# Kernel tuning notes

Measured on AMD Instinct MI355X. Metric: run time of the kernel, lower is better.

The kernel has to match this reference:

```python
import jax, jax.numpy as jnp
import numpy as np
import math

B, S, D, H = 2, 2048, 1024, 16
HD = D // H  # 64


def setup_inputs() -> dict:
    key = jax.random.key(0)
    ks = jax.random.split(key, 7)
    scale = 1.0 / math.sqrt(D)
    return {
        "hidden_states": jax.random.normal(ks[0], (B, S, D), jnp.float32),
        "attention_mask": jnp.zeros((B, 1, 1, S), jnp.int32),  # 0 = valid (code negates .bool())
        "Wq": jax.random.normal(ks[1], (D, D), jnp.float32) * scale,
        "bq": jnp.zeros((D,), jnp.float32),
        "Wk": jax.random.normal(ks[2], (D, D), jnp.float32) * scale,
        "bk": jnp.zeros((D,), jnp.float32),
        "Wv": jax.random.normal(ks[3], (D, D), jnp.float32) * scale,
        "bv": jnp.zeros((D,), jnp.float32),
    }


def reference(hidden_states, attention_mask, Wq, bq, Wk, bk, Wv, bv):
    b, s, d = hidden_states.shape

    def proj(W, bias):
        # torch Linear: x @ W.T + b ; weight shape [out, in]
        y = jnp.einsum('bsd,ed->bse', hidden_states, W) + bias
        return y.reshape(b, s, H, HD).transpose(0, 2, 1, 3)  # b h s d

    q, k, v = proj(Wq, bq), proj(Wk, bk), proj(Wv, bv)

    scores = jnp.einsum('bhqd,bhkd->bhqk', q, k) * (1.0 / math.sqrt(HD))
    causal = jnp.tril(jnp.ones((s, s), bool))[None, None]          # [1,1,S,S]
    pad = ~(attention_mask.astype(bool))                           # [B,1,1,S], True = valid
    mask = causal & pad
    scores = jnp.where(mask, scores, -jnp.inf)
    probs = jax.nn.softmax(scores, axis=-1)  # dropout prob = 0.0 -> identity
    out = jnp.einsum('bhqk,bhkd->bhqd', probs, v)
    return out.transpose(0, 2, 1, 3).reshape(b, s, d)
```

## Files before the change

kernel.cpp:

```cpp
#include <hip/hip_runtime.h>

typedef __bf16 bf16;
typedef __bf16 bf16x4 __attribute__((ext_vector_type(4)));
typedef __bf16 bf16x8 __attribute__((ext_vector_type(8)));
typedef float f32x4 __attribute__((ext_vector_type(4)));
typedef float f32x16 __attribute__((ext_vector_type(16)));
typedef unsigned u32x4 __attribute__((ext_vector_type(4)));

#define DEV __device__ __forceinline__

typedef const __attribute__((address_space(1))) void gvoid_t;
typedef __attribute__((address_space(3))) void lvoid_t;

DEV void gload_lds16(const void* g, void* l) {
  __builtin_amdgcn_global_load_lds((gvoid_t*)g, (lvoid_t*)l, 16, 0, 0);
}

DEV f32x4 mfma16(bf16x8 a, bf16x8 b, f32x4 c) {
  return __builtin_amdgcn_mfma_f32_16x16x32_bf16(a, b, c, 0, 0, 0);
}
DEV f32x16 mfma32(bf16x8 a, bf16x8 b, f32x16 c) {
  return __builtin_amdgcn_mfma_f32_32x32x16_bf16(a, b, c, 0, 0, 0);
}

DEV unsigned pk2(float lo, float hi) {
  unsigned r;
  asm("v_cvt_pk_bf16_f32 %0, %1, %2" : "=v"(r) : "v"(lo), "v"(hi));
  return r;
}

#define QSCALE 0.18033688011112042f

__global__ __launch_bounds__(256) void cvt_all(
    const float* __restrict__ hs, const float* __restrict__ Wq,
    const float* __restrict__ Wk, const float* __restrict__ Wv,
    bf16* __restrict__ Xb, bf16* __restrict__ Wb) {
  const int i = blockIdx.x * 256 + threadIdx.x;
  const float* src;
  bf16* dst;
  int off;
  if (i < 1048576) {
    src = hs; dst = Xb; off = i;
  } else {
    const int j = i - 1048576;
    const int sel = j >> 18;
    off = j & 262143;
    src = (sel == 0) ? Wq : (sel == 1) ? Wk : Wv;
    dst = Wb + (size_t)sel * 1048576;
  }
  float4 f = reinterpret_cast<const float4*>(src)[off];
  bf16x4 o;
  o[0] = (bf16)f.x; o[1] = (bf16)f.y; o[2] = (bf16)f.z; o[3] = (bf16)f.w;
  reinterpret_cast<bf16x4*>(dst)[off] = o;
}

__global__ __launch_bounds__(256) void gemm_qkv(
    const bf16* __restrict__ X, const bf16* __restrict__ W,
    const float* __restrict__ bq, const float* __restrict__ bk,
    const float* __restrict__ bv,
    bf16* __restrict__ Q, bf16* __restrict__ Kf, bf16* __restrict__ Vf) {
  __shared__ bf16 As[128 * 64];
  __shared__ bf16 Bs[128 * 64];
  const int t = threadIdx.x;
  const int lane = t & 63, w = t >> 6;
  const int wr = w >> 1, wc = w & 1;
  const int bid = blockIdx.x;
  const int swzb = (bid & 7) * 96 + (bid >> 3);
  const int m0 = (swzb / 24) * 128;
  const int n0 = (swzb % 24) * 128;
  const int cl = lane & 15, g8 = (lane >> 4) * 8;

  f32x4 acc[4][4];
  for (int mi = 0; mi < 4; ++mi)
    for (int ni = 0; ni < 4; ++ni)
      for (int r = 0; r < 4; ++r) acc[mi][ni][r] = 0.0f;

  for (int k0 = 0; k0 < 1024; k0 += 64) {
#pragma unroll
    for (int i = 0; i < 4; ++i) {
      int c = i * 256 + t;
      int row = c >> 3, col8 = (c & 7) * 8;
      gload_lds16(X + (size_t)(m0 + row) * 1024 + k0 + col8, As + c * 8);
      gload_lds16(W + (size_t)(n0 + row) * 1024 + k0 + col8, Bs + c * 8);
    }
    __syncthreads();
#pragma unroll
    for (int kk = 0; kk < 64; kk += 32) {
      bf16x8 a[4], b[4];
#pragma unroll
      for (int mi = 0; mi < 4; ++mi)
        a[mi] = *(const bf16x8*)&As[(wr * 64 + mi * 16 + cl) * 64 + kk + g8];
#pragma unroll
      for (int ni = 0; ni < 4; ++ni)
        b[ni] = *(const bf16x8*)&Bs[(wc * 64 + ni * 16 + cl) * 64 + kk + g8];
      __builtin_amdgcn_s_setprio(1);
#pragma unroll
      for (int mi = 0; mi < 4; ++mi)
#pragma unroll
        for (int ni = 0; ni < 4; ++ni)
          acc[mi][ni] = mfma16(a[mi], b[ni], acc[mi][ni]);
      __builtin_amdgcn_s_setprio(0);
    }
    __syncthreads();
  }

  const int rq = (lane >> 4) * 4;
#pragma unroll
  for (int mi = 0; mi < 4; ++mi) {
#pragma unroll
    for (int ni = 0; ni < 4; ++ni) {
      const int n = n0 + wc * 64 + ni * 16 + cl;
      const int mbase = m0 + wr * 64 + mi * 16 + rq;
      const int b = mbase >> 11, s0 = mbase & 2047;
      if (n < 1024) {
        const float bias = bq[n];
        const int h = n >> 6, hd = n & 63;
#pragma unroll
        for (int r = 0; r < 4; ++r)
          Q[(((size_t)(b * 16 + h)) * 2048 + s0 + r) * 64 + hd] =
              (bf16)((acc[mi][ni][r] + bias) * QSCALE);
      } else if (n < 2048) {
        const int n2 = n - 1024;
        const float bias = bk[n2];
        const int h = n2 >> 6, hd = n2 & 63;
        const int kt = s0 >> 6, half = (s0 >> 5) & 1, rr = s0 & 31;
        const size_t base =
            ((size_t)((b * 16 + h) * 32 + kt) * 8 + half * 4 + (hd >> 4)) * 512 +
            ((((hd >> 3) & 1) * 32 + rr) * 8 + (hd & 7));
#pragma unroll
        for (int r = 0; r < 4; ++r)
          Kf[base + r * 8] = (bf16)(acc[mi][ni][r] + bias);
      } else {
        const int n2 = n - 2048;
        const float bias = bv[n2];
        const int h = n2 >> 6, hd = n2 & 63;
        const int kt = s0 >> 6, half = (s0 >> 5) & 1;
        const int j = (s0 >> 4) & 1, hi2 = (s0 >> 3) & 1;
        const size_t idx =
            ((size_t)(((b * 16 + h) * 32 + kt) * 4 + half * 2 + j) * 2 +
             (hd >> 5)) * 512 +
            ((hi2 * 32 + (hd & 31)) * 8 + (s0 & 7));
        bf16x4 pk;
#pragma unroll
        for (int r = 0; r < 4; ++r) pk[r] = (bf16)(acc[mi][ni][r] + bias);
        *(bf16x4*)&Vf[idx] = pk;
      }
    }
  }
}

__global__ __launch_bounds__(256, 3) void flash_attn(
    const bf16* __restrict__ Q, const bf16* __restrict__ Kf,
    const bf16* __restrict__ Vf, const int* __restrict__ amask,
    float* __restrict__ out) {
  __shared__ float Oar[2][2048];
  __shared__ float Lar[2][32];
  __shared__ unsigned long long mk[32];
  const int t = threadIdx.x, lane = t & 63, w = t >> 6;
  const int bh = blockIdx.x & 31;
  const int p = blockIdx.x >> 5;
  const int b = bh >> 4, h = bh & 15;
  const int sub = w >> 1, par = w & 1;
  const int r31 = lane & 31, hi = lane >> 5;

  const bf16* Qp = Q + (size_t)bh * 2048 * 64;
  const bf16* Kfb = Kf + (size_t)bh * 32 * 4096 + lane * 8;
  const bf16* Vfb = Vf + (size_t)bh * 32 * 4096 + lane * 8;

#pragma unroll
  for (int i = 0; i < 8; ++i) {
    const int kt = w * 8 + i;
    const unsigned long long bal =
        __ballot(amask[b * 2048 + kt * 64 + lane] != 0);
    if (lane == 0) mk[kt] = bal;
  }
  __syncthreads();

  for (int sw = 0; sw < 2; ++sw) {
    const int qt = sw ? p : 31 - p;
    const int row0 = qt * 64 + sub * 32;
    bf16x8 qf[4];
#pragma unroll
    for (int hdk = 0; hdk < 4; ++hdk)
      qf[hdk] =
          *(const bf16x8*)&Qp[(size_t)(row0 + r31) * 64 + hdk * 16 + hi * 8];
    f32x16 o0, o1;
#pragma unroll
    for (int rg = 0; rg < 16; ++rg) { o0[rg] = 0.0f; o1[rg] = 0.0f; }
    float ls = 0.0f;

    for (int kt = par; kt <= qt; kt += 2) {
      const bf16* kb = Kfb + (size_t)kt * 4096;
      const bf16* vb = Vfb + (size_t)kt * 4096;
      bf16x8 kf[8], vf[8];
#pragma unroll
      for (int u = 0; u < 8; ++u) kf[u] = *(const bf16x8*)(kb + u * 512);
#pragma unroll
      for (int u = 0; u < 8; ++u) vf[u] = *(const bf16x8*)(vb + u * 512);
      const unsigned long long pb = mk[kt];
      const bool diag = (kt == qt);
      const bool domask = diag || (pb != 0ull);
      const int kv0 = kt * 64;
#pragma unroll
      for (int half = 0; half < 2; ++half) {
        f32x16 s4;
#pragma unroll
        for (int rg = 0; rg < 16; ++rg) s4[rg] = -12.0f;
        __builtin_amdgcn_s_setprio(1);
#pragma unroll
        for (int hdk = 0; hdk < 4; ++hdk)
          s4 = mfma32(kf[half * 4 + hdk], qf[hdk], s4);
        __builtin_amdgcn_s_setprio(0);
        if (domask) {
#pragma unroll
          for (int rg = 0; rg < 16; ++rg) {
            const int kvt = half * 32 + (rg & 3) + 8 * (rg >> 2) + 4 * hi;
            const bool bad = (diag && (kv0 + kvt > row0 + r31)) ||
                             ((pb >> kvt) & 1ull);
            s4[rg] = bad ? -1e30f : s4[rg];
          }
        }
        float pe[16];
#pragma unroll
        for (int rg = 0; rg < 16; ++rg) pe[rg] = exp2f(s4[rg]);
        ls += (((pe[0] + pe[1]) + (pe[2] + pe[3])) +
               ((pe[4] + pe[5]) + (pe[6] + pe[7]))) +
              (((pe[8] + pe[9]) + (pe[10] + pe[11])) +
               ((pe[12] + pe[13]) + (pe[14] + pe[15])));
#pragma unroll
        for (int j = 0; j < 2; ++j) {
          const unsigned a0 = pk2(pe[8 * j + 0], pe[8 * j + 1]);
          const unsigned a1 = pk2(pe[8 * j + 2], pe[8 * j + 3]);
          const unsigned b0 = pk2(pe[8 * j + 4], pe[8 * j + 5]);
          const unsigned b1 = pk2(pe[8 * j + 6], pe[8 * j + 7]);
          const unsigned xa0 = __shfl_xor(a0, 32, 64);
          const unsigned xa1 = __shfl_xor(a1, 32, 64);
          const unsigned xb0 = __shfl_xor(b0, 32, 64);
          const unsigned xb1 = __shfl_xor(b1, 32, 64);
          u32x4 wv;
          wv[0] = hi ? xb0 : a0;
          wv[1] = hi ? xb1 : a1;
          wv[2] = hi ? b0 : xa0;
          wv[3] = hi ? b1 : xa1;
          const bf16x8 paf = __builtin_bit_cast(bf16x8, wv);
          __builtin_amdgcn_s_setprio(1);
          o0 = mfma32(paf, vf[half * 4 + j * 2 + 0], o0);
          o1 = mfma32(paf, vf[half * 4 + j * 2 + 1], o1);
          __builtin_amdgcn_s_setprio(0);
        }
      }
    }

    ls += __shfl_xor(ls, 32, 64);
    if (par == 1) {
      float* Og = Oar[sub];
#pragma unroll
      for (int rg = 0; rg < 16; ++rg) {
        const int qrel = (rg & 3) + 8 * (rg >> 2) + 4 * hi;
        Og[qrel * 64 + r31] = o0[rg];
        Og[qrel * 64 + 32 + r31] = o1[rg];
      }
      if (lane < 32) Lar[sub][r31] = ls;
    }
    __syncthreads();
    if (par == 0) {
      const float lt = ls + Lar[sub][r31];
      const float inv = 1.0f / lt;
      const float* Og = Oar[sub];
#pragma unroll
      for (int rg = 0; rg < 16; ++rg) {
        const int qrel = (rg & 3) + 8 * (rg >> 2) + 4 * hi;
        const float invq = __shfl(inv, qrel, 64);
        float* op =
            &out[((size_t)b * 2048 + row0 + qrel) * 1024 + h * 64 + r31];
        op[0] = (o0[rg] + Og[qrel * 64 + r31]) * invq;
        op[32] = (o1[rg] + Og[qrel * 64 + 32 + r31]) * invq;
      }
    }
    __syncthreads();
  }
}

extern "C" void kernel_launch(void* const* d_in, const int* in_sizes, int n_in,
                              void* d_out, int out_size, void* d_ws,
                              size_t ws_size, hipStream_t stream) {
  const float* hs = (const float*)d_in[0];
  const int* amask = (const int*)d_in[1];
  const float* Wq = (const float*)d_in[2];
  const float* bq = (const float*)d_in[3];
  const float* Wk = (const float*)d_in[4];
  const float* bk = (const float*)d_in[5];
  const float* Wv = (const float*)d_in[6];
  const float* bv = (const float*)d_in[7];
  float* out = (float*)d_out;

  char* ws = (char*)d_ws;
  bf16* Xb = (bf16*)ws;
  bf16* Wb = (bf16*)(ws + 8ull * 1024 * 1024);
  bf16* Qb = (bf16*)(ws + 14ull * 1024 * 1024);
  bf16* Kfr = (bf16*)(ws + 22ull * 1024 * 1024);
  bf16* Vfr = (bf16*)(ws + 30ull * 1024 * 1024);

  cvt_all<<<7168, 256, 0, stream>>>(hs, Wq, Wk, Wv, Xb, Wb);
  gemm_qkv<<<768, 256, 0, stream>>>(Xb, Wb, bq, bk, bv, Qb, Kfr, Vfr);
  flash_attn<<<512, 256, 0, stream>>>(Qb, Kfr, Vfr, amask, out);
}
```

Baseline: 109.7 us.

## Split flash attention KV loop across four waves and double grid size

The attention kernel now gives each block one 32-row query sub-tile and splits the KV tiles across all four waves (stride 4) instead of two. The launch grows to 1024 blocks and occupancy is raised to 4 blocks per CU. Partial outputs are combined through a two-step LDS reduction. The bf16 P-matrix half swap now uses v_permlane32_swap instead of cross-lane shuffles, and exp2f is replaced by the hardware exp2 builtin. This trades more blocks and an extra reduction barrier for more parallelism over the causal KV range and fewer shuffle instructions.

Result: slower. 178.1 us (+62.4%).

```diff
diff --git a/kernel.cpp b/kernel.cpp
--- a/kernel.cpp
+++ b/kernel.cpp
@@ -27,6 +27,9 @@
   unsigned r;
   asm("v_cvt_pk_bf16_f32 %0, %1, %2" : "=v"(r) : "v"(lo), "v"(hi));
   return r;
+}
+DEV void plswap(unsigned& a, unsigned& b) {
+  asm("v_permlane32_swap_b32 %0, %1" : "+v"(a), "+v"(b));
 }
 
 #define QSCALE 0.18033688011112042f
@@ -149,7 +152,7 @@
   }
 }
 
-__global__ __launch_bounds__(256, 3) void flash_attn(
+__global__ __launch_bounds__(256, 4) void flash_attn(
     const bf16* __restrict__ Q, const bf16* __restrict__ Kf,
     const bf16* __restrict__ Vf, const int* __restrict__ amask,
     float* __restrict__ out) {
@@ -158,9 +161,9 @@
   __shared__ unsigned long long mk[32];
   const int t = threadIdx.x, lane = t & 63, w = t >> 6;
   const int bh = blockIdx.x & 31;
-  const int p = blockIdx.x >> 5;
+  const int p = (blockIdx.x >> 5) & 15;
+  const int sub = blockIdx.x >> 9;
   const int b = bh >> 4, h = bh & 15;
-  const int sub = w >> 1, par = w & 1;
   const int r31 = lane & 31, hi = lane >> 5;
 
   const bf16* Qp = Q + (size_t)bh * 2048 * 64;
@@ -176,6 +179,26 @@
   }
   __syncthreads();
 
+#define DUMPO(SL)                                                       \
+  do {                                                                  \
+    _Pragma("unroll") for (int rg = 0; rg < 16; ++rg) {                 \
+      const int qrel = (rg & 3) + 8 * (rg >> 2) + 4 * hi;               \
+      Oar[SL][qrel * 64 + r31] = o0[rg];                                \
+      Oar[SL][qrel * 64 + 32 + r31] = o1[rg];                           \
+    }                                                                   \
+    if (lane < 32) Lar[SL][r31] = ls;                                   \
+  } while (0)
+
+#define ADDO(SL)                                                        \
+  do {                                                                  \
+    _Pragma("unroll") for (int rg = 0; rg < 16; ++rg) {                 \
+      const int qrel = (rg & 3) + 8 * (rg >> 2) + 4 * hi;               \
+      o0[rg] += Oar[SL][qrel * 64 + r31];                               \
+      o1[rg] += Oar[SL][qrel * 64 + 32 + r31];                          \
+    }                                                                   \
+    ls += Lar[SL][r31];                                                 \
+  } while (0)
+
   for (int sw = 0; sw < 2; ++sw) {
     const int qt = sw ? p : 31 - p;
     const int row0 = qt * 64 + sub * 32;
@@ -189,7 +212,7 @@
     for (int rg = 0; rg < 16; ++rg) { o0[rg] = 0.0f; o1[rg] = 0.0f; }
     float ls = 0.0f;
 
-    for (int kt = par; kt <= qt; kt += 2) {
+    for (int kt = w; kt <= qt; kt += 4) {
       const bf16* kb = Kfb + (size_t)kt * 4096;
       const bf16* vb = Vfb + (size_t)kt * 4096;
       bf16x8 kf[8], vf[8];
@@ -222,26 +245,22 @@
         }
         float pe[16];
 #pragma unroll
-        for (int rg = 0; rg < 16; ++rg) pe[rg] = exp2f(s4[rg]);
+        for (int rg = 0; rg < 16; ++rg)
+          pe[rg] = __builtin_amdgcn_exp2f(s4[rg]);
         ls += (((pe[0] + pe[1]) + (pe[2] + pe[3])) +
                ((pe[4] + pe[5]) + (pe[6] + pe[7]))) +
               (((pe[8] + pe[9]) + (pe[10] + pe[11])) +
                ((pe[12] + pe[13]) + (pe[14] + pe[15])));
 #pragma unroll
         for (int j = 0; j < 2; ++j) {
-          const unsigned a0 = pk2(pe[8 * j + 0], pe[8 * j + 1]);
-          const unsigned a1 = pk2(pe[8 * j + 2], pe[8 * j + 3]);
-          const unsigned b0 = pk2(pe[8 * j + 4], pe[8 * j + 5]);
-          const unsigned b1 = pk2(pe[8 * j + 6], pe[8 * j + 7]);
-          const unsigned xa0 = __shfl_xor(a0, 32, 64);
-          const unsigned xa1 = __shfl_xor(a1, 32, 64);
-          const unsigned xb0 = __shfl_xor(b0, 32, 64);
-          const unsigned xb1 = __shfl_xor(b1, 32, 64);
+          unsigned a0 = pk2(pe[8 * j + 0], pe[8 * j + 1]);
+          unsigned a1 = pk2(pe[8 * j + 2], pe[8 * j + 3]);
+          unsigned b0 = pk2(pe[8 * j + 4], pe[8 * j + 5]);
+          unsigned b1 = pk2(pe[8 * j + 6], pe[8 * j + 7]);
+          plswap(a0, b0);
+          plswap(a1, b1);
           u32x4 wv;
-          wv[0] = hi ? xb0 : a0;
-          wv[1] = hi ? xb1 : a1;
-          wv[2] = hi ? b0 : xa0;
-          wv[3] = hi ? b1 : xa1;
+          wv[0] = a0; wv[1] = a1; wv[2] = b0; wv[3] = b1;
           const bf16x8 paf = __builtin_bit_cast(bf16x8, wv);
           __builtin_amdgcn_s_setprio(1);
           o0 = mfma32(paf, vf[half * 4 + j * 2 + 0], o0);
@@ -251,34 +270,34 @@
       }
     }
 
-    ls += __shfl_xor(ls, 32, 64);
-    if (par == 1) {
-      float* Og = Oar[sub];
-#pragma unroll
-      for (int rg = 0; rg < 16; ++rg) {
-        const int qrel = (rg & 3) + 8 * (rg >> 2) + 4 * hi;
-        Og[qrel * 64 + r31] = o0[rg];
-        Og[qrel * 64 + 32 + r31] = o1[rg];
-      }
-      if (lane < 32) Lar[sub][r31] = ls;
-    }
-    __syncthreads();
-    if (par == 0) {
-      const float lt = ls + Lar[sub][r31];
-      const float inv = 1.0f / lt;
-      const float* Og = Oar[sub];
+    {
+      unsigned la = __builtin_bit_cast(unsigned, ls), lb = la;
+      plswap(la, lb);
+      ls = __builtin_bit_cast(float, la) + __builtin_bit_cast(float, lb);
+    }
+    if (w == 2) DUMPO(0);
+    if (w == 3) DUMPO(1);
+    __syncthreads();
+    if (w == 0) ADDO(0);
+    if (w == 1) { ADDO(1); DUMPO(1); }
+    __syncthreads();
+    if (w == 0) {
+      ADDO(1);
+      const float inv = 1.0f / ls;
 #pragma unroll
       for (int rg = 0; rg < 16; ++rg) {
         const int qrel = (rg & 3) + 8 * (rg >> 2) + 4 * hi;
         const float invq = __shfl(inv, qrel, 64);
         float* op =
             &out[((size_t)b * 2048 + row0 + qrel) * 1024 + h * 64 + r31];
-        op[0] = (o0[rg] + Og[qrel * 64 + r31]) * invq;
-        op[32] = (o1[rg] + Og[qrel * 64 + 32 + r31]) * invq;
+        op[0] = o0[rg] * invq;
+        op[32] = o1[rg] * invq;
       }
     }
     __syncthreads();
   }
+#undef DUMPO
+#undef ADDO
 }
 
 extern "C" void kernel_launch(void* const* d_in, const int* in_sizes, int n_in,
@@ -303,5 +322,5 @@
 
   cvt_all<<<7168, 256, 0, stream>>>(hs, Wq, Wk, Wv, Xb, Wb);
   gemm_qkv<<<768, 256, 0, stream>>>(Xb, Wb, bq, bk, bv, Qb, Kfr, Vfr);
-  flash_attn<<<512, 256, 0, stream>>>(Qb, Kfr, Vfr, amask, out);
-}
+  flash_attn<<<1024, 256, 0, stream>>>(Qb, Kfr, Vfr, amask, out);
+}
```
